# Kernel tuning notes

Measured on AMD Instinct MI355X. Metric: run time of the kernel, lower is better.

## Reference

```python
import jax, jax.numpy as jnp
import numpy as np

N = 50000      # nodes
E = 800000     # edges
D_IN = 128
D_OUT = 128
R = 8          # relation types
EPS = 1e-12    # F.normalize eps


def setup_inputs() -> dict:
    key = jax.random.key(0)
    ks = jax.random.split(key, 10)
    s_in = 1.0 / np.sqrt(D_IN)
    s_out = 1.0 / np.sqrt(D_OUT)
    return {
        "x": jax.random.normal(ks[0], (N, D_IN), jnp.float32),
        "W1": jax.random.normal(ks[1], (R, D_IN, D_OUT), jnp.float32) * s_in,
        "loopW1": jax.random.normal(ks[2], (D_IN, D_OUT), jnp.float32) * s_in,
        "b1": jax.random.normal(ks[3], (D_OUT,), jnp.float32) * 0.01,
        "W2": jax.random.normal(ks[4], (R, D_OUT, D_OUT), jnp.float32) * s_out,
        "loopW2": jax.random.normal(ks[5], (D_OUT, D_OUT), jnp.float32) * s_out,
        "b2": jax.random.normal(ks[6], (D_OUT,), jnp.float32) * 0.01,
        "src": jax.random.randint(ks[7], (E,), 0, N),
        "dst": jax.random.randint(ks[8], (E,), 0, N),
        "etypes": jax.random.randint(ks[9], (E,), 0, R),
    }


def rel_layer(x, src, dst, etypes, W, loopW, b):
    # transform every node by every relation: [R, N, D_out]
    xw = jnp.einsum('ni,rio->rno', x, W)
    # gather per-edge messages: [E, D_out]
    msg = xw[etypes, src]
    # scatter-add to destination nodes
    agg = jax.ops.segment_sum(msg, dst, num_segments=x.shape[0])
    # self-loop + bias (DGL RelGraphConv defaults)
    return agg + x @ loopW + b


def reference(x, W1, loopW1, b1, W2, loopW2, b2, src, dst, etypes):
    h = jax.nn.relu(rel_layer(x, src, dst, etypes, W1, loopW1, b1))
    h = rel_layer(h, src, dst, etypes, W2, loopW2, b2)
    # F.normalize: row-wise L2, eps=1e-12
    nrm = jnp.maximum(jnp.linalg.norm(h, axis=1, keepdims=True), EPS)
    return h / nrm
```

## Files before the change

kernel.cpp:

```cpp
#include <hip/hip_runtime.h>
#include <hip/hip_bf16.h>

#define D 128
#define CH 4096

typedef unsigned int u32;
typedef unsigned short u16;
typedef __attribute__((ext_vector_type(8))) short s16x8;
typedef __attribute__((ext_vector_type(4))) float f32x4;
typedef __attribute__((ext_vector_type(2))) float f32x2;
typedef __attribute__((ext_vector_type(2))) u32 u32x2;

__device__ __forceinline__ float bf2f(u16 u) {
    union { u32 u; float f; } v; v.u = ((u32)u) << 16; return v.f;
}
__device__ __forceinline__ u16 f2bf(float f) {
    union { float f; u32 u; } v; v.f = f;
    return (u16)((v.u + 0x7fffu + ((v.u >> 16) & 1u)) >> 16);
}
__device__ __forceinline__ u32 pack_bf2(float a, float b) {
    __hip_bfloat162 t = __float22bfloat162_rn(make_float2(a, b));
    union { __hip_bfloat162 t; u32 u; } v; v.t = t; return v.u;
}
__device__ __forceinline__ void unpack2(u32 u, float& lo, float& hi) {
    union { u32 u; float f; } a, b;
    a.u = u << 16; b.u = u & 0xffff0000u;
    lo = a.f; hi = b.f;
}

__global__ void detect_dtype(const u16* __restrict__ x, int* __restrict__ flag,
                             int* __restrict__ gcnt, int nbuck) {
    __shared__ int cnt;
    if (threadIdx.x == 0) cnt = 0;
    __syncthreads();
    if ((int)threadIdx.x < nbuck) gcnt[threadIdx.x] = 0;
    u16 u = x[2 * threadIdx.x];
    int e = (u >> 7) & 0xFF;
    if (e >= 96 && e <= 150) atomicAdd(&cnt, 1);
    __syncthreads();
    if (threadIdx.x == 0) *flag = (cnt >= 128) ? 0 : 1;
}

__global__ __launch_bounds__(256)
void to_bf16_all(const void* __restrict__ s0, const void* __restrict__ s1,
                 const void* __restrict__ s2, const void* __restrict__ s3,
                 const void* __restrict__ s4, const void* __restrict__ s5,
                 const void* __restrict__ s6,
                 u16* __restrict__ d0, u16* __restrict__ d1, u16* __restrict__ d2,
                 u16* __restrict__ d3, u16* __restrict__ d4, u16* __restrict__ d5,
                 u16* __restrict__ d6,
                 long long n0, long long n1, long long n2, long long n3,
                 long long n4, long long n5, long long n6,
                 const int* __restrict__ flag)
{
    if (*flag == 0) return;
    long long i = (long long)blockIdx.x * 256 + threadIdx.x;
    const void* s; u16* d; long long off;
    if      (i < n0)                   { s = s0; d = d0; off = i; }
    else if (i < n0+n1)                { s = s1; d = d1; off = i-n0; }
    else if (i < n0+n1+n2)             { s = s2; d = d2; off = i-n0-n1; }
    else if (i < n0+n1+n2+n3)          { s = s3; d = d3; off = i-n0-n1-n2; }
    else if (i < n0+n1+n2+n3+n4)       { s = s4; d = d4; off = i-n0-n1-n2-n3; }
    else if (i < n0+n1+n2+n3+n4+n5)    { s = s5; d = d5; off = i-n0-n1-n2-n3-n4; }
    else if (i < n0+n1+n2+n3+n4+n5+n6) { s = s6; d = d6; off = i-n0-n1-n2-n3-n4-n5; }
    else return;
    d[off] = f2bf(((const float*)s)[off]);
}

__global__ __launch_bounds__(256)
void csr_count(const int* __restrict__ dst, int* __restrict__ gcnt, int E, int nbuck) {
    __shared__ int scnt[256];
    int tid = threadIdx.x;
    scnt[tid] = 0;
    __syncthreads();
    int base = blockIdx.x * CH;
#pragma unroll
    for (int it = 0; it < CH / 256; ++it) {
        int e = base + it * 256 + tid;
        if (e < E) atomicAdd(&scnt[dst[e] >> 8], 1);
    }
    __syncthreads();
    if (tid < nbuck && scnt[tid] > 0) atomicAdd(&gcnt[tid], scnt[tid]);
}

__global__ __launch_bounds__(256)
void csr_scan(const int* __restrict__ gcnt, int* __restrict__ bstart, int* __restrict__ bcur,
              int nbuck, int N_, int E_, int* __restrict__ offs) {
    __shared__ int wpart[4];
    int tid = threadIdx.x, lane = tid & 63, wid = tid >> 6;
    int v = (tid < nbuck) ? gcnt[tid] : 0;
    int s = v;
#pragma unroll
    for (int off = 1; off < 64; off <<= 1) {
        int t = __shfl_up(s, off, 64);
        if (lane >= off) s += t;
    }
    if (lane == 63) wpart[wid] = s;
    __syncthreads();
    int add = 0;
    for (int w = 0; w < wid; ++w) add += wpart[w];
    int excl = add + s - v;
    if (tid <= nbuck) bstart[tid] = excl;
    if (tid < nbuck)  bcur[tid]  = excl;
    if (tid == 0) offs[N_] = E_;
}

__global__ __launch_bounds__(256)
void csr_part(const int* __restrict__ src, const int* __restrict__ dst,
              const int* __restrict__ et, int* __restrict__ bcur,
              u32* __restrict__ ebuf, int E, int N, int nbuck) {
    __shared__ int scnt[256], sbase[256];
    int tid = threadIdx.x;
    scnt[tid] = 0;
    __syncthreads();
    int base = blockIdx.x * CH;
#pragma unroll
    for (int it = 0; it < CH / 256; ++it) {
        int e = base + it * 256 + tid;
        if (e < E) atomicAdd(&scnt[dst[e] >> 8], 1);
    }
    __syncthreads();
    if (tid < nbuck) {
        int c = scnt[tid];
        sbase[tid] = c ? atomicAdd(&bcur[tid], c) : 0;
    }
    __syncthreads();
    scnt[tid] = 0;
    __syncthreads();
#pragma unroll
    for (int it = 0; it < CH / 256; ++it) {
        int e = base + it * 256 + tid;
        if (e >= E) continue;
        int d = dst[e];
        int b = d >> 8;
        int p = sbase[b] + atomicAdd(&scnt[b], 1);
        ebuf[p] = ((u32)(d & 255) << 24) | (u32)(et[e] * N + src[e]);
    }
}

__global__ __launch_bounds__(256)
void csr_emit(const u32* __restrict__ ebuf, const int* __restrict__ bstart,
              int* __restrict__ offs, int* __restrict__ rowidx, int N) {
    __shared__ int hist[256], excl[256], cur[256];
    __shared__ int wpart[4];
    int b = blockIdx.x, tid = threadIdx.x;
    int lo = bstart[b], hi = bstart[b + 1];
    hist[tid] = 0; cur[tid] = 0;
    __syncthreads();
    for (int i = lo + tid; i < hi; i += 256) atomicAdd(&hist[ebuf[i] >> 24], 1);
    __syncthreads();
    int lane = tid & 63, wid = tid >> 6;
    int v = hist[tid], s = v;
#pragma unroll
    for (int off = 1; off < 64; off <<= 1) {
        int t = __shfl_up(s, off, 64);
        if (lane >= off) s += t;
    }
    if (lane == 63) wpart[wid] = s;
    __syncthreads();
    int add = 0;
    for (int w = 0; w < wid; ++w) add += wpart[w];
    int e_ = add + s - v;
    excl[tid] = e_;
    int node = (b << 8) + tid;
    if (node < N) offs[node] = lo + e_;
    __syncthreads();
    for (int i = lo + tid; i < hi; i += 256) {
        u32 rec = ebuf[i];
        int dl = rec >> 24;
        int p = lo + excl[dl] + atomicAdd(&cur[dl], 1);
        rowidx[p] = (int)(rec & 0xFFFFFFu);
    }
}

__global__ __launch_bounds__(256)
void gemm_k128(const u16* __restrict__ Ac, const u16* __restrict__ Ao,
               const u16* __restrict__ Wc, const u16* __restrict__ Wo,
               const u16* __restrict__ lWc, const u16* __restrict__ lWo,
               const u16* __restrict__ bc, const u16* __restrict__ bo,
               const int* __restrict__ flag,
               int M, int R_, u16* __restrict__ xw, u16* __restrict__ sl)
{
    __shared__ u16 As[128 * 128];
    const bool f = (*flag != 0);
    const u16* A     = f ? Ac  : Ao;
    const u16* Wall  = f ? Wc  : Wo;
    const u16* loopW = f ? lWc : lWo;
    const u16* bias  = f ? bc  : bo;

    const int y = blockIdx.y;
    const u16* B = (y < R_) ? (Wall + (long long)y * D * D) : loopW;
    const int row0 = blockIdx.x * 128;
    const int tid  = threadIdx.x;
    const int lane = tid & 63;
    const int wv   = tid >> 6;
    const int quad = lane >> 4;
    const int l16  = lane & 15;

    {
        int r_base = (wv << 2) + (lane >> 4);
        int c      = lane & 15;
        auto* lds0 = (__attribute__((address_space(3))) char*)As;
#pragma unroll
        for (int it = 0; it < 8; ++it) {
            int rl = it * 16 + r_base;
            int cg = c ^ (rl & 15);
            int rg = row0 + rl; if (rg >= M) rg = M - 1;
            const u16* gp = A + (long long)rg * D + cg * 8;
            __builtin_amdgcn_global_load_lds(
                (const __attribute__((address_space(1))) void*)gp,
                (__attribute__((address_space(3))) void*)(lds0 + it * 4096 + wv * 1024),
                16, 0, 0);
        }
    }

    s16x8 bf[4][2];
#pragma unroll
    for (int kk = 0; kk < 4; ++kk)
#pragma unroll
        for (int j = 0; j < 8; ++j) {
            u32 p = *(const u32*)(B + (kk * 32 + quad * 8 + j) * D + wv * 32 + 2 * l16);
            bf[kk][0][j] = (short)(p & 0xffffu);
            bf[kk][1][j] = (short)(p >> 16);
        }

    f32x4 acc[8][2];
#pragma unroll
    for (int mt = 0; mt < 8; ++mt) { acc[mt][0] = (f32x4)0.f; acc[mt][1] = (f32x4)0.f; }

    __syncthreads();

#pragma unroll
    for (int kk = 0; kk < 4; ++kk) {
        const int chunk = (kk * 4 + quad) ^ l16;
#pragma unroll
        for (int mt = 0; mt < 8; ++mt) {
            int rl = mt * 16 + l16;
            s16x8 a = *(const s16x8*)(As + rl * D + chunk * 8);
            acc[mt][0] = __builtin_amdgcn_mfma_f32_16x16x32_bf16(a, bf[kk][0], acc[mt][0], 0, 0, 0);
            acc[mt][1] = __builtin_amdgcn_mfma_f32_16x16x32_bf16(a, bf[kk][1], acc[mt][1], 0, 0, 0);
        }
    }

    long long MD64 = (long long)M * 64;
    int cpair = wv * 16 + l16;
    if (y < R_) {
        u32* o = (u32*)xw + (long long)y * MD64;
#pragma unroll
        for (int mt = 0; mt < 8; ++mt)
#pragma unroll
            for (int i = 0; i < 4; ++i) {
                int r = row0 + mt * 16 + quad * 4 + i;
                if (r >= M) continue;
                o[(long long)r * 64 + cpair] = pack_bf2(acc[mt][0][i], acc[mt][1][i]);
            }
    } else {
        float b0 = bf2f(bias[wv * 32 + 2 * l16]);
        float b1 = bf2f(bias[wv * 32 + 2 * l16 + 1]);
        u32* o = (u32*)sl;
#pragma unroll
        for (int mt = 0; mt < 8; ++mt)
#pragma unroll
            for (int i = 0; i < 4; ++i) {
                int r = row0 + mt * 16 + quad * 4 + i;
                if (r >= M) continue;
                o[(long long)r * 64 + cpair] = pack_bf2(acc[mt][0][i] + b0, acc[mt][1][i] + b1);
            }
    }
}

__global__ __launch_bounds__(256)
void aggregate(const u16* __restrict__ xw, const u16* __restrict__ sl,
               const int* __restrict__ offs, const int* __restrict__ rowidx,
               void* __restrict__ out, int N, int mode, const int* __restrict__ flag)
{
    int node = blockIdx.x * 4 + (threadIdx.x >> 6);
    int lane = threadIdx.x & 63;
    int p  = lane & 31;
    int hi = lane >> 5;
    if (node >= N) return;
    const u32x2* xw2 = (const u32x2*)xw;

    float a0, a1, a2, a3;
    if (hi == 0) {
        u32x2 s2 = ((const u32x2*)sl)[(long long)node * 32 + p];
        unpack2(s2[0], a0, a1);
        unpack2(s2[1], a2, a3);
    } else { a0 = a1 = a2 = a3 = 0.f; }

    int j = offs[node], j1 = offs[node + 1];
    for (; j + 8 <= j1; j += 8) {
        int r0 = rowidx[j + 0 + hi];
        int r1 = rowidx[j + 2 + hi];
        int r2 = rowidx[j + 4 + hi];
        int r3 = rowidx[j + 6 + hi];
        u32x2 u0 = xw2[(long long)r0 * 32 + p];
        u32x2 u1 = xw2[(long long)r1 * 32 + p];
        u32x2 u2 = xw2[(long long)r2 * 32 + p];
        u32x2 u3 = xw2[(long long)r3 * 32 + p];
        float l, h;
        unpack2(u0[0], l, h); a0 += l; a1 += h;  unpack2(u0[1], l, h); a2 += l; a3 += h;
        unpack2(u1[0], l, h); a0 += l; a1 += h;  unpack2(u1[1], l, h); a2 += l; a3 += h;
        unpack2(u2[0], l, h); a0 += l; a1 += h;  unpack2(u2[1], l, h); a2 += l; a3 += h;
        unpack2(u3[0], l, h); a0 += l; a1 += h;  unpack2(u3[1], l, h); a2 += l; a3 += h;
    }
    for (; j < j1; j += 2) {
        bool ok = (j + hi < j1);
        int rr = rowidx[ok ? j + hi : j];
        u32x2 u = xw2[(long long)rr * 32 + p];
        if (!ok) { u[0] = 0; u[1] = 0; }
        float l, h;
        unpack2(u[0], l, h); a0 += l; a1 += h;
        unpack2(u[1], l, h); a2 += l; a3 += h;
    }

    a0 += __shfl_xor(a0, 32, 64);
    a1 += __shfl_xor(a1, 32, 64);
    a2 += __shfl_xor(a2, 32, 64);
    a3 += __shfl_xor(a3, 32, 64);

    if (mode == 0) {
        if (hi == 0) {
            u32x2 w;
            w[0] = pack_bf2(fmaxf(a0, 0.f), fmaxf(a1, 0.f));
            w[1] = pack_bf2(fmaxf(a2, 0.f), fmaxf(a3, 0.f));
            ((u32x2*)out)[(long long)node * 32 + p] = w;
        }
    } else {
        float s = a0 * a0 + a1 * a1 + a2 * a2 + a3 * a3;
#pragma unroll
        for (int off = 16; off > 0; off >>= 1) s += __shfl_xor(s, off, 64);
        float sc = 1.f / fmaxf(sqrtf(s), 1e-12f);
        if (hi == 0) {
            if (*flag) {
                f32x4 w; w[0] = a0 * sc; w[1] = a1 * sc; w[2] = a2 * sc; w[3] = a3 * sc;
                ((f32x4*)out)[(long long)node * 32 + p] = w;
            } else {
                u32x2 w;
                w[0] = pack_bf2(a0 * sc, a1 * sc);
                w[1] = pack_bf2(a2 * sc, a3 * sc);
                ((u32x2*)out)[(long long)node * 32 + p] = w;
            }
        }
    }
}

static inline size_t align256(size_t x) { return (x + 255) & ~(size_t)255; }

extern "C" void kernel_launch(void* const* d_in, const int* in_sizes, int n_in,
                              void* d_out, int out_size, void* d_ws, size_t ws_size,
                              hipStream_t stream)
{
    const void* x_in   = d_in[0];
    const void* W1_in  = d_in[1];
    const void* lW1_in = d_in[2];
    const void* b1_in  = d_in[3];
    const void* W2_in  = d_in[4];
    const void* lW2_in = d_in[5];
    const void* b2_in  = d_in[6];
    const int* src = (const int*)d_in[7];
    const int* dst = (const int*)d_in[8];
    const int* et  = (const int*)d_in[9];

    const int N = in_sizes[0] / D;
    const int E = in_sizes[7];
    const int R = in_sizes[1] / (D * D);
    const int nbuck = (N + 255) >> 8;

    const long long ND  = (long long)N * D;
    const long long RDD = (long long)R * D * D;
    const long long DDl = (long long)D * D;

    size_t off = 0;
    auto alloc = [&](size_t bytes) { size_t o = off; off = align256(off + bytes); return o; };
    size_t o_flag = alloc(256);
    size_t o_xc   = alloc((size_t)ND * 2);
    size_t o_W1   = alloc((size_t)RDD * 2);
    size_t o_lW1  = alloc((size_t)DDl * 2);
    size_t o_b1   = alloc((size_t)D * 2);
    size_t o_W2   = alloc((size_t)RDD * 2);
    size_t o_lW2  = alloc((size_t)DDl * 2);
    size_t o_b2   = alloc((size_t)D * 2);
    size_t o_sl   = alloc((size_t)ND * 2);
    size_t o_h    = alloc((size_t)ND * 2);
    size_t o_offs = alloc((size_t)(N + 1) * 4);
    size_t o_gcnt = alloc(1024);
    size_t o_bst  = alloc(1040 * 4);
    size_t o_bcur = alloc(1024);
    size_t o_ebuf = alloc((size_t)E * 4);
    size_t o_ridx = alloc((size_t)E * 4);
    size_t o_xw   = alloc((size_t)R * ND * 2);
    (void)ws_size;

    char* ws = (char*)d_ws;
    int* flag   = (int*)(ws + o_flag);
    u16* x_c    = (u16*)(ws + o_xc);
    u16* W1c    = (u16*)(ws + o_W1);
    u16* lW1c   = (u16*)(ws + o_lW1);
    u16* b1c    = (u16*)(ws + o_b1);
    u16* W2c    = (u16*)(ws + o_W2);
    u16* lW2c   = (u16*)(ws + o_lW2);
    u16* b2c    = (u16*)(ws + o_b2);
    u16* sl     = (u16*)(ws + o_sl);
    u16* h      = (u16*)(ws + o_h);
    int* offs   = (int*)(ws + o_offs);
    int* gcnt   = (int*)(ws + o_gcnt);
    int* bstart = (int*)(ws + o_bst);
    int* bcur   = (int*)(ws + o_bcur);
    u32* ebuf   = (u32*)(ws + o_ebuf);
    int* rowidx = (int*)(ws + o_ridx);
    u16* xw     = (u16*)(ws + o_xw);

    dim3 blk(256, 1, 1);
    int mb    = (N + 127) / 128;
    int nblkE = (E + CH - 1) / CH;
    auto cdiv = [](long long n) { return (u32)((n + 255) / 256); };

    detect_dtype<<<dim3(1), blk, 0, stream>>>((const u16*)x_in, flag, gcnt, nbuck);
    long long tot = ND + RDD + DDl + D + RDD + DDl + D;
    to_bf16_all<<<dim3(cdiv(tot)), blk, 0, stream>>>(
        x_in, W1_in, lW1_in, b1_in, W2_in, lW2_in, b2_in,
        x_c, W1c, lW1c, b1c, W2c, lW2c, b2c,
        ND, RDD, DDl, (long long)D, RDD, DDl, (long long)D, flag);

    csr_count<<<dim3(nblkE), blk, 0, stream>>>(dst, gcnt, E, nbuck);
    csr_scan<<<dim3(1), blk, 0, stream>>>(gcnt, bstart, bcur, nbuck, N, E, offs);
    csr_part<<<dim3(nblkE), blk, 0, stream>>>(src, dst, et, bcur, ebuf, E, N, nbuck);
    csr_emit<<<dim3(nbuck), blk, 0, stream>>>(ebuf, bstart, offs, rowidx, N);

    gemm_k128<<<dim3(mb, R + 1), blk, 0, stream>>>(
        x_c, (const u16*)x_in, W1c, (const u16*)W1_in, lW1c, (const u16*)lW1_in,
        b1c, (const u16*)b1_in, flag, N, R, xw, sl);
    aggregate<<<dim3((N + 3) / 4), blk, 0, stream>>>(xw, sl, offs, rowidx, h, N, 0, flag);

    gemm_k128<<<dim3(mb, R + 1), blk, 0, stream>>>(
        h, h, W2c, (const u16*)W2_in, lW2c, (const u16*)lW2_in,
        b2c, (const u16*)b2_in, flag, N, R, xw, sl);
    aggregate<<<dim3((N + 3) / 4), blk, 0, stream>>>(xw, sl, offs, rowidx, d_out, N, 1, flag);
}
```

Baseline: 292.0 us.

## Aggregate raw features per relation before GEMM, fuse relation GEMMs with epilogue

Reorders each layer as sum_r (A_r x) W_r: a new gather kernel sums neighbour input rows into per-relation bf16 planes, then one fused GEMM kernel loops over all relations plus the self-loop, accumulating in registers and applying bias, ReLU or L2 normalization in its epilogue. This removes the separate aggregate pass and the per-edge gather of 128-wide transformed rows from the R×N×D xw buffer. In exchange it writes and reads R planes of N×D aggregated features, packs src into 16 bits (valid only while N < 65536), and does the per-lane relation selection with a switch.

```diff
diff --git a/kernel.cpp b/kernel.cpp
--- a/kernel.cpp
+++ b/kernel.cpp
@@ -3,13 +3,13 @@
 
 #define D 128
 #define CH 4096
+#define BM 64
 
 typedef unsigned int u32;
 typedef unsigned short u16;
 typedef __attribute__((ext_vector_type(8))) short s16x8;
 typedef __attribute__((ext_vector_type(4))) float f32x4;
 typedef __attribute__((ext_vector_type(2))) float f32x2;
-typedef __attribute__((ext_vector_type(2))) u32 u32x2;
 
 __device__ __forceinline__ float bf2f(u16 u) {
     union { u32 u; float f; } v; v.u = ((u32)u) << 16; return v.f;
@@ -134,7 +134,7 @@
         int d = dst[e];
         int b = d >> 8;
         int p = sbase[b] + atomicAdd(&scnt[b], 1);
-        ebuf[p] = ((u32)(d & 255) << 24) | (u32)(et[e] * N + src[e]);
+        ebuf[p] = ((u32)(d & 255) << 24) | ((u32)et[e] << 16) | (u32)src[e];
     }
 }
 
@@ -173,175 +173,197 @@
     }
 }
 
-__global__ __launch_bounds__(256)
-void gemm_k128(const u16* __restrict__ Ac, const u16* __restrict__ Ao,
-               const u16* __restrict__ Wc, const u16* __restrict__ Wo,
-               const u16* __restrict__ lWc, const u16* __restrict__ lWo,
-               const u16* __restrict__ bc, const u16* __restrict__ bo,
-               const int* __restrict__ flag,
-               int M, int R_, u16* __restrict__ xw, u16* __restrict__ sl)
+#define ACC8(et_, u_) do { float l_, h_; unpack2((u_), l_, h_);        \
+    switch (et_) {                                                     \
+    case 0: aL[0] += l_; aH[0] += h_; break;                           \
+    case 1: aL[1] += l_; aH[1] += h_; break;                           \
+    case 2: aL[2] += l_; aH[2] += h_; break;                           \
+    case 3: aL[3] += l_; aH[3] += h_; break;                           \
+    case 4: aL[4] += l_; aH[4] += h_; break;                           \
+    case 5: aL[5] += l_; aH[5] += h_; break;                           \
+    case 6: aL[6] += l_; aH[6] += h_; break;                           \
+    default: aL[7] += l_; aH[7] += h_; break; } } while (0)
+
+__global__ __launch_bounds__(256)
+void agg_pre(const u16* __restrict__ xc, const u16* __restrict__ xo,
+             const int* __restrict__ offs, const int* __restrict__ rowidx,
+             u16* __restrict__ s, int N_, int R_, const int* __restrict__ flag)
 {
-    __shared__ u16 As[128 * 128];
+    const u16* x = (*flag != 0) ? xc : xo;
+    int node = blockIdx.x * 4 + (threadIdx.x >> 6);
+    int lane = threadIdx.x & 63;
+    if (node >= N_) return;
+    const u32* xr = (const u32*)x;
+
+    float aL[8] = {0.f,0.f,0.f,0.f,0.f,0.f,0.f,0.f};
+    float aH[8] = {0.f,0.f,0.f,0.f,0.f,0.f,0.f,0.f};
+
+    int j  = __builtin_amdgcn_readfirstlane(offs[node]);
+    int j1 = __builtin_amdgcn_readfirstlane(offs[node + 1]);
+
+    for (; j + 4 <= j1; j += 4) {
+        int v0 = __builtin_amdgcn_readfirstlane(rowidx[j + 0]);
+        int v1 = __builtin_amdgcn_readfirstlane(rowidx[j + 1]);
+        int v2 = __builtin_amdgcn_readfirstlane(rowidx[j + 2]);
+        int v3 = __builtin_amdgcn_readfirstlane(rowidx[j + 3]);
+        u32 u0 = xr[(size_t)(v0 & 0xffff) * 64 + lane];
+        u32 u1 = xr[(size_t)(v1 & 0xffff) * 64 + lane];
+        u32 u2 = xr[(size_t)(v2 & 0xffff) * 64 + lane];
+        u32 u3 = xr[(size_t)(v3 & 0xffff) * 64 + lane];
+        ACC8(v0 >> 16, u0);
+        ACC8(v1 >> 16, u1);
+        ACC8(v2 >> 16, u2);
+        ACC8(v3 >> 16, u3);
+    }
+    for (; j < j1; ++j) {
+        int v = __builtin_amdgcn_readfirstlane(rowidx[j]);
+        u32 u = xr[(size_t)(v & 0xffff) * 64 + lane];
+        ACC8(v >> 16, u);
+    }
+
+    size_t plane = (size_t)N_ * 64;
+    u32* sp = (u32*)s + (size_t)node * 64 + lane;
+#pragma unroll
+    for (int r = 0; r < 8; ++r)
+        if (r < R_) sp[(size_t)r * plane] = pack_bf2(aL[r], aH[r]);
+}
+
+__global__ __launch_bounds__(256)
+void gemm_fused(const u16* __restrict__ s,
+                const u16* __restrict__ selfc, const u16* __restrict__ selfo,
+                const u16* __restrict__ Wc, const u16* __restrict__ Wo,
+                const u16* __restrict__ lWc, const u16* __restrict__ lWo,
+                const u16* __restrict__ bc, const u16* __restrict__ bo,
+                const int* __restrict__ flag,
+                int M, int R_, int mode, void* __restrict__ out)
+{
+    __shared__ u16 As[BM * 128];
     const bool f = (*flag != 0);
-    const u16* A     = f ? Ac  : Ao;
+    const u16* self  = f ? selfc : selfo;
     const u16* Wall  = f ? Wc  : Wo;
     const u16* loopW = f ? lWc : lWo;
     const u16* bias  = f ? bc  : bo;
 
-    const int y = blockIdx.y;
-    const u16* B = (y < R_) ? (Wall + (long long)y * D * D) : loopW;
-    const int row0 = blockIdx.x * 128;
+    const int row0 = blockIdx.x * BM;
     const int tid  = threadIdx.x;
     const int lane = tid & 63;
     const int wv   = tid >> 6;
     const int quad = lane >> 4;
     const int l16  = lane & 15;
 
-    {
-        int r_base = (wv << 2) + (lane >> 4);
-        int c      = lane & 15;
-        auto* lds0 = (__attribute__((address_space(3))) char*)As;
-#pragma unroll
-        for (int it = 0; it < 8; ++it) {
-            int rl = it * 16 + r_base;
-            int cg = c ^ (rl & 15);
-            int rg = row0 + rl; if (rg >= M) rg = M - 1;
-            const u16* gp = A + (long long)rg * D + cg * 8;
-            __builtin_amdgcn_global_load_lds(
-                (const __attribute__((address_space(1))) void*)gp,
-                (__attribute__((address_space(3))) void*)(lds0 + it * 4096 + wv * 1024),
-                16, 0, 0);
+    f32x4 acc[4][2];
+#pragma unroll
+    for (int mt = 0; mt < 4; ++mt) { acc[mt][0] = (f32x4)0.f; acc[mt][1] = (f32x4)0.f; }
+
+    const size_t planeE = (size_t)M * D;
+    const int r_base = (wv << 2) + (lane >> 4);
+    const int ccol   = lane & 15;
+
+    for (int c = 0; c <= R_; ++c) {
+        const u16* Ak = (c < R_) ? (s + (size_t)c * planeE) : self;
+        const u16* B  = (c < R_) ? (Wall + (size_t)c * D * D) : loopW;
+
+        {
+            auto* lds0 = (__attribute__((address_space(3))) char*)As;
+            int cg = ccol ^ r_base;
+            int rg0 = row0 + r_base;
+#pragma unroll
+            for (int it = 0; it < 4; ++it) {
+                int rg = rg0 + it * 16; if (rg >= M) rg = M - 1;
+                const u16* gp = Ak + (size_t)rg * D + cg * 8;
+                __builtin_amdgcn_global_load_lds(
+                    (const __attribute__((address_space(1))) void*)gp,
+                    (__attribute__((address_space(3))) void*)(lds0 + it * 4096 + wv * 1024),
+                    16, 0, 0);
+            }
         }
-    }
-
-    s16x8 bf[4][2];
-#pragma unroll
-    for (int kk = 0; kk < 4; ++kk)
-#pragma unroll
-        for (int j = 0; j < 8; ++j) {
-            u32 p = *(const u32*)(B + (kk * 32 + quad * 8 + j) * D + wv * 32 + 2 * l16);
-            bf[kk][0][j] = (short)(p & 0xffffu);
-            bf[kk][1][j] = (short)(p >> 16);
+
+        s16x8 bf[4][2];
+#pragma unroll
+        for (int ks = 0; ks < 4; ++ks)
+#pragma unroll
+            for (int jj = 0; jj < 8; ++jj) {
+                u32 p = *(const u32*)(B + (ks * 32 + quad * 8 + jj) * D + wv * 32 + 2 * l16);
+                bf[ks][0][jj] = (short)(p & 0xffffu);
+                bf[ks][1][jj] = (short)(p >> 16);
+            }
+
+        __syncthreads();
+
+#pragma unroll
+        for (int ks = 0; ks < 4; ++ks) {
+            const int chunk = (ks * 4 + quad) ^ l16;
+#pragma unroll
+            for (int mt = 0; mt < 4; ++mt) {
+                s16x8 a = *(const s16x8*)(As + (mt * 16 + l16) * D + chunk * 8);
+                acc[mt][0] = __builtin_amdgcn_mfma_f32_16x16x32_bf16(a, bf[ks][0], acc[mt][0], 0, 0, 0);
+                acc[mt][1] = __builtin_amdgcn_mfma_f32_16x16x32_bf16(a, bf[ks][1], acc[mt][1], 0, 0, 0);
+            }
         }
-
-    f32x4 acc[8][2];
-#pragma unroll
-    for (int mt = 0; mt < 8; ++mt) { acc[mt][0] = (f32x4)0.f; acc[mt][1] = (f32x4)0.f; }
-
-    __syncthreads();
-
-#pragma unroll
-    for (int kk = 0; kk < 4; ++kk) {
-        const int chunk = (kk * 4 + quad) ^ l16;
-#pragma unroll
-        for (int mt = 0; mt < 8; ++mt) {
-            int rl = mt * 16 + l16;
-            s16x8 a = *(const s16x8*)(As + rl * D + chunk * 8);
-            acc[mt][0] = __builtin_amdgcn_mfma_f32_16x16x32_bf16(a, bf[kk][0], acc[mt][0], 0, 0, 0);
-            acc[mt][1] = __builtin_amdgcn_mfma_f32_16x16x32_bf16(a, bf[kk][1], acc[mt][1], 0, 0, 0);
-        }
-    }
-
-    long long MD64 = (long long)M * 64;
-    int cpair = wv * 16 + l16;
-    if (y < R_) {
-        u32* o = (u32*)xw + (long long)y * MD64;
-#pragma unroll
-        for (int mt = 0; mt < 8; ++mt)
+        __syncthreads();
+    }
+
+    const int cpair = wv * 16 + l16;
+    const float b0 = bf2f(bias[2 * cpair]);
+    const float b1 = bf2f(bias[2 * cpair + 1]);
+
+    if (mode == 0) {
+        u32* o = (u32*)out;
+#pragma unroll
+        for (int mt = 0; mt < 4; ++mt)
 #pragma unroll
             for (int i = 0; i < 4; ++i) {
                 int r = row0 + mt * 16 + quad * 4 + i;
                 if (r >= M) continue;
-                o[(long long)r * 64 + cpair] = pack_bf2(acc[mt][0][i], acc[mt][1][i]);
+                o[(size_t)r * 64 + cpair] = pack_bf2(fmaxf(acc[mt][0][i] + b0, 0.f),
+                                                     fmaxf(acc[mt][1][i] + b1, 0.f));
             }
     } else {
-        float b0 = bf2f(bias[wv * 32 + 2 * l16]);
-        float b1 = bf2f(bias[wv * 32 + 2 * l16 + 1]);
-        u32* o = (u32*)sl;
-#pragma unroll
-        for (int mt = 0; mt < 8; ++mt)
+        float pr[4][4];
+#pragma unroll
+        for (int mt = 0; mt < 4; ++mt)
 #pragma unroll
             for (int i = 0; i < 4; ++i) {
-                int r = row0 + mt * 16 + quad * 4 + i;
+                float a0 = acc[mt][0][i] + b0;
+                float a1 = acc[mt][1][i] + b1;
+                acc[mt][0][i] = a0; acc[mt][1][i] = a1;
+                float p = a0 * a0 + a1 * a1;
+                p += __shfl_xor(p, 1, 64);
+                p += __shfl_xor(p, 2, 64);
+                p += __shfl_xor(p, 4, 64);
+                p += __shfl_xor(p, 8, 64);
+                pr[mt][i] = p;
+            }
+        float* fs = (float*)As;
+        if (l16 == 0) {
+#pragma unroll
+            for (int mt = 0; mt < 4; ++mt)
+#pragma unroll
+                for (int i = 0; i < 4; ++i)
+                    fs[(mt * 16 + quad * 4 + i) * 4 + wv] = pr[mt][i];
+        }
+        __syncthreads();
+        if (tid < 64) {
+            float ssum = fs[tid * 4] + fs[tid * 4 + 1] + fs[tid * 4 + 2] + fs[tid * 4 + 3];
+            fs[256 + tid] = 1.f / fmaxf(sqrtf(ssum), 1e-12f);
+        }
+        __syncthreads();
+#pragma unroll
+        for (int mt = 0; mt < 4; ++mt)
+#pragma unroll
+            for (int i = 0; i < 4; ++i) {
+                int rl = mt * 16 + quad * 4 + i;
+                int r = row0 + rl;
                 if (r >= M) continue;
-                o[(long long)r * 64 + cpair] = pack_bf2(acc[mt][0][i] + b0, acc[mt][1][i] + b1);
-            }
-    }
-}
-
-__global__ __launch_bounds__(256)
-void aggregate(const u16* __restrict__ xw, const u16* __restrict__ sl,
-               const int* __restrict__ offs, const int* __restrict__ rowidx,
-               void* __restrict__ out, int N, int mode, const int* __restrict__ flag)
-{
-    int node = blockIdx.x * 4 + (threadIdx.x >> 6);
-    int lane = threadIdx.x & 63;
-    int p  = lane & 31;
-    int hi = lane >> 5;
-    if (node >= N) return;
-    const u32x2* xw2 = (const u32x2*)xw;
-
-    float a0, a1, a2, a3;
-    if (hi == 0) {
-        u32x2 s2 = ((const u32x2*)sl)[(long long)node * 32 + p];
-        unpack2(s2[0], a0, a1);
-        unpack2(s2[1], a2, a3);
-    } else { a0 = a1 = a2 = a3 = 0.f; }
-
-    int j = offs[node], j1 = offs[node + 1];
-    for (; j + 8 <= j1; j += 8) {
-        int r0 = rowidx[j + 0 + hi];
-        int r1 = rowidx[j + 2 + hi];
-        int r2 = rowidx[j + 4 + hi];
-        int r3 = rowidx[j + 6 + hi];
-        u32x2 u0 = xw2[(long long)r0 * 32 + p];
-        u32x2 u1 = xw2[(long long)r1 * 32 + p];
-        u32x2 u2 = xw2[(long long)r2 * 32 + p];
-        u32x2 u3 = xw2[(long long)r3 * 32 + p];
-        float l, h;
-        unpack2(u0[0], l, h); a0 += l; a1 += h;  unpack2(u0[1], l, h); a2 += l; a3 += h;
-        unpack2(u1[0], l, h); a0 += l; a1 += h;  unpack2(u1[1], l, h); a2 += l; a3 += h;
-        unpack2(u2[0], l, h); a0 += l; a1 += h;  unpack2(u2[1], l, h); a2 += l; a3 += h;
-        unpack2(u3[0], l, h); a0 += l; a1 += h;  unpack2(u3[1], l, h); a2 += l; a3 += h;
-    }
-    for (; j < j1; j += 2) {
-        bool ok = (j + hi < j1);
-        int rr = rowidx[ok ? j + hi : j];
-        u32x2 u = xw2[(long long)rr * 32 + p];
-        if (!ok) { u[0] = 0; u[1] = 0; }
-        float l, h;
-        unpack2(u[0], l, h); a0 += l; a1 += h;
-        unpack2(u[1], l, h); a2 += l; a3 += h;
-    }
-
-    a0 += __shfl_xor(a0, 32, 64);
-    a1 += __shfl_xor(a1, 32, 64);
-    a2 += __shfl_xor(a2, 32, 64);
-    a3 += __shfl_xor(a3, 32, 64);
-
-    if (mode == 0) {
-        if (hi == 0) {
-            u32x2 w;
-            w[0] = pack_bf2(fmaxf(a0, 0.f), fmaxf(a1, 0.f));
-            w[1] = pack_bf2(fmaxf(a2, 0.f), fmaxf(a3, 0.f));
-            ((u32x2*)out)[(long long)node * 32 + p] = w;
-        }
-    } else {
-        float s = a0 * a0 + a1 * a1 + a2 * a2 + a3 * a3;
-#pragma unroll
-        for (int off = 16; off > 0; off >>= 1) s += __shfl_xor(s, off, 64);
-        float sc = 1.f / fmaxf(sqrtf(s), 1e-12f);
-        if (hi == 0) {
-            if (*flag) {
-                f32x4 w; w[0] = a0 * sc; w[1] = a1 * sc; w[2] = a2 * sc; w[3] = a3 * sc;
-                ((f32x4*)out)[(long long)node * 32 + p] = w;
-            } else {
-                u32x2 w;
-                w[0] = pack_bf2(a0 * sc, a1 * sc);
-                w[1] = pack_bf2(a2 * sc, a3 * sc);
-                ((u32x2*)out)[(long long)node * 32 + p] = w;
-            }
-        }
+                float sc = fs[256 + rl];
+                float a0 = acc[mt][0][i] * sc, a1 = acc[mt][1][i] * sc;
+                if (f) {
+                    f32x2 w; w[0] = a0; w[1] = a1;
+                    ((f32x2*)out)[(size_t)r * 64 + cpair] = w;
+                } else {
+                    ((u32*)out)[(size_t)r * 64 + cpair] = pack_bf2(a0, a1);
+                }
+            }
     }
 }
 
@@ -381,7 +403,6 @@
     size_t o_W2   = alloc((size_t)RDD * 2);
     size_t o_lW2  = alloc((size_t)DDl * 2);
     size_t o_b2   = alloc((size_t)D * 2);
-    size_t o_sl   = alloc((size_t)ND * 2);
     size_t o_h    = alloc((size_t)ND * 2);
     size_t o_offs = alloc((size_t)(N + 1) * 4);
     size_t o_gcnt = alloc(1024);
@@ -389,7 +410,7 @@
     size_t o_bcur = alloc(1024);
     size_t o_ebuf = alloc((size_t)E * 4);
     size_t o_ridx = alloc((size_t)E * 4);
-    size_t o_xw   = alloc((size_t)R * ND * 2);
+    size_t o_s    = alloc((size_t)R * ND * 2);
     (void)ws_size;
 
     char* ws = (char*)d_ws;
@@ -401,7 +422,6 @@
     u16* W2c    = (u16*)(ws + o_W2);
     u16* lW2c   = (u16*)(ws + o_lW2);
     u16* b2c    = (u16*)(ws + o_b2);
-    u16* sl     = (u16*)(ws + o_sl);
     u16* h      = (u16*)(ws + o_h);
     int* offs   = (int*)(ws + o_offs);
     int* gcnt   = (int*)(ws + o_gcnt);
@@ -409,10 +429,10 @@
     int* bcur   = (int*)(ws + o_bcur);
     u32* ebuf   = (u32*)(ws + o_ebuf);
     int* rowidx = (int*)(ws + o_ridx);
-    u16* xw     = (u16*)(ws + o_xw);
+    u16* sbuf   = (u16*)(ws + o_s);
 
     dim3 blk(256, 1, 1);
-    int mb    = (N + 127) / 128;
+    int mb    = (N + BM - 1) / BM;
     int nblkE = (E + CH - 1) / CH;
     auto cdiv = [](long long n) { return (u32)((n + 255) / 256); };
 
@@ -428,13 +448,15 @@
     csr_part<<<dim3(nblkE), blk, 0, stream>>>(src, dst, et, bcur, ebuf, E, N, nbuck);
     csr_emit<<<dim3(nbuck), blk, 0, stream>>>(ebuf, bstart, offs, rowidx, N);
 
-    gemm_k128<<<dim3(mb, R + 1), blk, 0, stream>>>(
-        x_c, (const u16*)x_in, W1c, (const u16*)W1_in, lW1c, (const u16*)lW1_in,
-        b1c, (const u16*)b1_in, flag, N, R, xw, sl);
-    aggregate<<<dim3((N + 3) / 4), blk, 0, stream>>>(xw, sl, offs, rowidx, h, N, 0, flag);
-
-    gemm_k128<<<dim3(mb, R + 1), blk, 0, stream>>>(
-        h, h, W2c, (const u16*)W2_in, lW2c, (const u16*)lW2_in,
-        b2c, (const u16*)b2_in, flag, N, R, xw, sl);
-    aggregate<<<dim3((N + 3) / 4), blk, 0, stream>>>(xw, sl, offs, rowidx, d_out, N, 1, flag);
-}
+    agg_pre<<<dim3((N + 3) / 4), blk, 0, stream>>>(
+        x_c, (const u16*)x_in, offs, rowidx, sbuf, N, R, flag);
+    gemm_fused<<<dim3(mb), blk, 0, stream>>>(
+        sbuf, x_c, (const u16*)x_in, W1c, (const u16*)W1_in, lW1c, (const u16*)lW1_in,
+        b1c, (const u16*)b1_in, flag, N, R, 0, h);
+
+    agg_pre<<<dim3((N + 3) / 4), blk, 0, stream>>>(
+        h, h, offs, rowidx, sbuf, N, R, flag);
+    gemm_fused<<<dim3(mb), blk, 0, stream>>>(
+        sbuf, h, h, W2c, (const u16*)W2_in, lW2c, (const u16*)lW2_in,
+        b2c, (const u16*)b2_in, flag, N, R, 1, d_out);
+}
```

After: 317.4 us. +8.7%, slower.
